# Kernel tuning notes

Measured on AMD Instinct MI355X. Metric: run time of the kernel, lower is better.

The kernel has to match this reference:

```python
import jax, jax.numpy as jnp
import numpy as np
from jax import lax

NUM_CLASSES = 80
CONF_THRE = 0.01   # testconf in source
NMS_THRE = 0.2     # nmsthresh in source
N = 8400           # YOLOX anchors at 640x640: 80^2+40^2+20^2
IMG = 640.0


def setup_inputs() -> dict:
    key = jax.random.key(0)
    pred = jax.random.uniform(key, (N, 5 + NUM_CLASSES), dtype=jnp.float32)
    # scale cx,cy,w,h to pixel units so boxes are realistic
    pred = pred.at[:, :4].multiply(IMG)
    return {"prediction": pred}


def _pairwise_iou(boxes):
    # boxes: [N,4] in x1,y1,x2,y2
    area = (boxes[:, 2] - boxes[:, 0]) * (boxes[:, 3] - boxes[:, 1])  # [N]
    lt = jnp.maximum(boxes[:, None, :2], boxes[None, :, :2])  # [N,N,2]
    rb = jnp.minimum(boxes[:, None, 2:], boxes[None, :, 2:])  # [N,N,2]
    wh = jnp.clip(rb - lt, 0.0)
    inter = wh[..., 0] * wh[..., 1]
    return inter / (area[:, None] + area[None, :] - inter + 1e-9)


def reference(prediction):
    # ---- box corner decode (cx,cy,w,h -> x1,y1,x2,y2) ----
    cx, cy, w, h = prediction[:, 0], prediction[:, 1], prediction[:, 2], prediction[:, 3]
    boxes = jnp.stack([cx - w / 2, cy - h / 2, cx + w / 2, cy + h / 2], axis=1)

    # ---- per-class max ----
    cls_scores = prediction[:, 5:5 + NUM_CLASSES]
    class_conf = jnp.max(cls_scores, axis=1, keepdims=True)            # [N,1]
    class_pred = jnp.argmax(cls_scores, axis=1).astype(prediction.dtype)[:, None]

    obj = prediction[:, 4]
    valid = obj >= CONF_THRE                                            # conf mask

    # detections = [x1,y1,x2,y2, obj_conf, class_conf, class_pred]  -> [N,7]
    det = jnp.concatenate([boxes, obj[:, None], class_conf, class_pred], axis=1)

    # ---- class-agnostic greedy NMS on obj score (fixed-shape version) ----
    scores = jnp.where(valid, obj, -1.0)
    order = jnp.argsort(-scores)
    det_s = det[order]
    boxes_s = boxes[order]
    valid_s = valid[order]

    iou = _pairwise_iou(boxes_s)  # [N,N] ~282MB, dominant traffic
    idx = jnp.arange(N)

    def step(keep, inp):
        i, row, v = inp
        alive = keep[i] & v                      # only a kept valid box suppresses
        supp = alive & (row > NMS_THRE) & (idx > i)
        return keep & ~supp, None

    keep0 = jnp.ones((N,), dtype=bool)
    keep, _ = lax.scan(step, keep0, (idx, iou, valid_s))
    keep = keep & valid_s

    # suppressed / below-conf rows are zeroed (torch returns a ragged subset;
    # here we return the score-sorted, mask-zeroed fixed-shape equivalent)
    out = det_s * keep[:, None].astype(det_s.dtype)
    return out
```

## Files before the change

kernel.cpp:

```cpp
#include <hip/hip_runtime.h>
#include <stdint.h>

#define N_BOX 8400
#define NCLS 80
#define PSTRIDE 85
#define NW 132
#define NTILE 8778
#define ZROWI N_BOX
#define CONF_T 0.01f
#define NMS_T 0.2f

typedef unsigned long long u64;

#define OFF_DET     0
#define OFF_DIAGT   0
#define OFF_SUP1    67584
#define OFF_SUP2    135168
#define OFF_SUP3    202752
#define OFF_KEYS    268800
#define OFF_DETS    336000
#define OFF_BOXESS  604800
#define OFF_MASK    739200
#define OFF_VCNT    9611712

__device__ __forceinline__ unsigned fmap_desc(float f) {
    unsigned u = __float_as_uint(f);
    unsigned m = (u & 0x80000000u) ? ~u : (u | 0x80000000u);
    return ~m;
}

__device__ __forceinline__ u64 readlane64(u64 v, int lane) {
    unsigned lo = (unsigned)__builtin_amdgcn_readlane((int)(unsigned)v, lane);
    unsigned hi = (unsigned)__builtin_amdgcn_readlane((int)(unsigned)(v >> 32), lane);
    return ((u64)hi << 32) | lo;
}

__device__ __forceinline__ u64 shfl_xor64(u64 v, int m) {
    int lo = __shfl_xor((int)(unsigned)v, m);
    int hi = __shfl_xor((int)(unsigned)(v >> 32), m);
    return ((u64)(unsigned)hi << 32) | (unsigned)lo;
}

__device__ __forceinline__ u64 bittranspose64(u64 x, int lane) {
    const u64 P0 = 0x5555555555555555ull, P1 = 0x3333333333333333ull,
              P2 = 0x0F0F0F0F0F0F0F0Full, P3 = 0x00FF00FF00FF00FFull,
              P4 = 0x0000FFFF0000FFFFull, P5 = 0x00000000FFFFFFFFull;
#define TSTEP(s, p) do {                                                 \
        u64 y = shfl_xor64(x, s);                                        \
        x = (lane & (s)) ? ((x & ~(p)) | ((y & ~(p)) >> (s)))            \
                         : ((x & (p))  | ((y & (p))  << (s)));           \
    } while (0)
    TSTEP(1, P0); TSTEP(2, P1); TSTEP(4, P2);
    TSTEP(8, P3); TSTEP(16, P4); TSTEP(32, P5);
#undef TSTEP
    return x;
}

__device__ __forceinline__ u64 wmask(int w, int V) {
    int nb = V - (w << 6);
    if (nb <= 0) return 0ull;
    if (nb >= 64) return ~0ull;
    return (1ull << nb) - 1ull;
}

__device__ __forceinline__ void step_barrier() {
    asm volatile("s_waitcnt lgkmcnt(0)" ::: "memory");
    __builtin_amdgcn_s_barrier();
    asm volatile("" ::: "memory");
}

__global__ __launch_bounds__(256) void prep_k(const float* __restrict__ pred,
                                              float* __restrict__ det,
                                              u64* __restrict__ keys,
                                              u64* __restrict__ mask) {
    if (blockIdx.x == 0 && threadIdx.x < NW)
        mask[(size_t)ZROWI * NW + threadIdx.x] = 0ull;
    int gt = blockIdx.x * 256 + threadIdx.x;
    int i = gt >> 2, q = gt & 3;
    if (i >= N_BOX) return;
    const float* p = pred + (size_t)i * PSTRIDE;
    int cbase = q * 20;
    float best = p[5 + cbase];
    int arg = cbase;
    for (int c = 1; c < 20; ++c) {
        float v = p[5 + cbase + c];
        if (v > best) { best = v; arg = cbase + c; }
    }
    for (int d = 1; d < 4; d <<= 1) {
        float ob = __shfl_xor(best, d);
        int   oa = __shfl_xor(arg, d);
        if (ob > best || (ob == best && oa < arg)) { best = ob; arg = oa; }
    }
    if (q == 0) {
        float cx = p[0], cy = p[1], w = p[2], h = p[3], obj = p[4];
        float hw = __fmul_rn(w, 0.5f), hh = __fmul_rn(h, 0.5f);
        float x1 = __fsub_rn(cx, hw), y1 = __fsub_rn(cy, hh);
        float x2 = __fadd_rn(cx, hw), y2 = __fadd_rn(cy, hh);
        bool valid = (obj >= CONF_T);
        float score = valid ? obj : -1.0f;
        keys[i] = ((u64)fmap_desc(score) << 32) | (unsigned)i;
        float4* dr = (float4*)(det + (size_t)i * 8);
        dr[0] = make_float4(x1, y1, x2, y2);
        dr[1] = make_float4(obj, best, (float)arg, 0.0f);
    }
}

__global__ __launch_bounds__(256) void rank_k(const u64* __restrict__ keys,
                                              const float* __restrict__ det,
                                              float4* __restrict__ det_s,
                                              float4* __restrict__ boxes_s,
                                              int* __restrict__ vcount) {
    int t = threadIdx.x;
    int i = blockIdx.x * 32 + (t & 31);
    int s = t >> 5;
    u64 my = (i < N_BOX) ? keys[i] : ~0ull;
    int cnt = 0, cv = 0;
    int j0 = s * 1050, j1 = j0 + 1050;
    for (int j = j0; j < j1; j += 2) {
        ulonglong2 kk = *(const ulonglong2*)(keys + j);
        cnt += (kk.x < my) + (kk.y < my);
        cv  += ((long long)kk.x >= 0) + ((long long)kk.y >= 0);
    }
    __shared__ int sc[256], sv[256];
    sc[t] = cnt; sv[t] = cv;
    __syncthreads();
    if (t < 32) {
        int r = sc[t] + sc[t + 32] + sc[t + 64] + sc[t + 96]
              + sc[t + 128] + sc[t + 160] + sc[t + 192] + sc[t + 224];
        if (i < N_BOX) {
            const float4* dr = (const float4*)(det + (size_t)i * 8);
            float4 b0 = dr[0], b1 = dr[1];
            det_s[(size_t)r * 2]     = b0;
            det_s[(size_t)r * 2 + 1] = b1;
            boxes_s[r] = b0;
        }
        if (blockIdx.x == 0 && t == 0) {
            *vcount = sv[0] + sv[32] + sv[64] + sv[96]
                    + sv[128] + sv[160] + sv[192] + sv[224];
        }
    }
}

__global__ __launch_bounds__(256) void mask_k(const float4* __restrict__ boxes_s,
                                              u64* __restrict__ mask,
                                              u64* __restrict__ diagT,
                                              u64* __restrict__ sup1,
                                              u64* __restrict__ sup2,
                                              u64* __restrict__ sup3) {
    int sub = threadIdx.x >> 6, lane = threadIdx.x & 63;
    int tt = blockIdx.x * 4 + sub;
    bool tv = (tt < NTILE);
    __shared__ float4 cB[4][64];
    __shared__ float  cA[4][64];
    int rb = 0, cb = 0;
    if (tv) {
        rb = (int)((2.0f * NW + 1.0f
                    - sqrtf((2.0f * NW + 1.0f) * (2.0f * NW + 1.0f) - 8.0f * (float)tt)) * 0.5f);
        while (rb > 0 && rb * NW - rb * (rb - 1) / 2 > tt) rb--;
        while ((rb + 1) * NW - (rb + 1) * rb / 2 <= tt) rb++;
        cb = rb + (tt - (rb * NW - rb * (rb - 1) / 2));
        int c0 = cb * 64 + lane;
        float4 b = (c0 < N_BOX) ? boxes_s[c0] : make_float4(0.f, 0.f, 0.f, 0.f);
        cB[sub][lane] = b;
        cA[sub][lane] = __fmul_rn(__fsub_rn(b.z, b.x), __fsub_rn(b.w, b.y));
    }
    __syncthreads();
    if (!tv) return;
    int r = rb * 64 + lane;
    bool inb = (r < N_BOX);
    float4 rx = boxes_s[inb ? r : (N_BOX - 1)];
    float ra = __fmul_rn(__fsub_rn(rx.z, rx.x), __fsub_rn(rx.w, rx.y));
    u64 bits = 0ull;
    int cbase = cb * 64;
    for (int j = 0; j < 64; ++j) {
        int c = cbase + j;
        if (c >= N_BOX || c <= r) continue;
        float4 cx4 = cB[sub][j];
        float ltx = fmaxf(rx.x, cx4.x), lty = fmaxf(rx.y, cx4.y);
        float rbx = fminf(rx.z, cx4.z), rby = fminf(rx.w, cx4.w);
        float wx = fmaxf(__fsub_rn(rbx, ltx), 0.0f);
        float wy = fmaxf(__fsub_rn(rby, lty), 0.0f);
        float inter = __fmul_rn(wx, wy);
        float denom = __fadd_rn(__fsub_rn(__fadd_rn(ra, cA[sub][j]), inter), 1e-9f);
        float iou = __fdiv_rn(inter, denom);
        if (iou > NMS_T) bits |= (1ull << j);
    }
    if (inb) mask[(size_t)r * NW + cb] = bits;
    int d = cb - rb;
    if (d <= 3) {
        u64 tb = bittranspose64(bits, lane);
        size_t idx = (size_t)cb * 64 + lane;
        if (d == 0)      diagT[idx] = tb;
        else if (d == 1) sup1[idx]  = tb;
        else if (d == 2) sup2[idx]  = tb;
        else             sup3[idx]  = tb;
    }
}

__global__ __launch_bounds__(256, 1) void scan_k(const u64* __restrict__ mask,
                                                 const u64* __restrict__ diagT,
                                                 const u64* __restrict__ sup1,
                                                 const u64* __restrict__ sup2,
                                                 const u64* __restrict__ sup3,
                                                 const int* __restrict__ vcount,
                                                 const float* __restrict__ det_s,
                                                 float* __restrict__ out) {
    __shared__ u64 remvP1[NW + 2];
    __shared__ u64 remvP2[NW + 2];
    __shared__ u64 Lbuf[NW];
    int tid = threadIdx.x, lane = tid & 63, wv = tid >> 6;
    int V = *vcount;
    for (int i = tid; i < NW + 2; i += 256) { remvP1[i] = 0ull; remvP2[i] = 0ull; }
    __syncthreads();

    if (wv == 0) {
        u64 A1 = 0ull, A2 = 0ull, A3 = 0ull;
        u64 d0P, s1P, s2P, s3P, d0Q, s1Q, s2Q, s3Q;
#define TL(S, kk) do {                                                   \
        int t_ = (kk) < NW ? (kk) : (NW - 1);                            \
        size_t ix_ = (size_t)t_ * 64 + lane;                             \
        d0##S = diagT[ix_]; s1##S = sup1[ix_];                           \
        s2##S = sup2[ix_];  s3##S = sup3[ix_];                           \
    } while (0)
#define STEP0(kk, S) do {                                                \
        int k_ = (kk);                                                   \
        u64 cur_ = remvP1[k_] | remvP2[k_];                              \
        cur_ |= __ballot((s1##S & A1) != 0ull);                          \
        cur_ |= __ballot((s2##S & A2) != 0ull);                          \
        cur_ |= __ballot((s3##S & A3) != 0ull);                          \
        u64 m_ = wmask(k_, V);                                           \
        u64 ns_ = (~cur_) & m_;                                          \
        u64 L_ = 0ull;                                                   \
        while (ns_) {                                                    \
            int b_ = __builtin_ctzll(ns_);                               \
            L_ |= 1ull << b_;                                            \
            u64 sup_ = __ballot((int)((d0##S >> b_) & 1ull));            \
            ns_ &= ~sup_;                                                \
            ns_ &= ~(1ull << b_);                                        \
        }                                                                \
        if (lane == 0) Lbuf[k_] = L_;                                    \
        A3 = A2; A2 = A1; A1 = L_;                                       \
        TL(S, k_ + 2);                                                   \
        step_barrier();                                                  \
    } while (0)
        TL(P, 0);
        TL(Q, 1);
        for (int c = 0; c < NW; c += 2) {
            STEP0(c + 0, P);
            STEP0(c + 1, Q);
        }
#undef STEP0
#undef TL
    } else if (wv <= 2) {
        int half = wv - 1;
        u64* myP = half ? remvP2 : remvP1;
        int tw = (lane < 4) ? (128 + lane) : 131;
        u64 Ra = 0ull, Rb = 0ull, Rc = 0ull;
        u64 Pa0=0,Pa1=0,Pa2=0,Pa3=0, Pb0=0,Pb1=0,Pb2=0,Pb3=0, Pc0=0,Pc1=0,Pc2=0,Pc3=0;
        u64 Qa0=0,Qa1=0,Qa2=0,Qa3=0, Qb0=0,Qb1=0,Qb2=0,Qb3=0, Qc0=0,Qc1=0,Qc2=0,Qc3=0;

#define CONS(S) do {                                                     \
        Ra |= (S##a0 | S##a1) | (S##a2 | S##a3);                         \
        Rb |= (S##b0 | S##b1) | (S##b2 | S##b3);                         \
        Rc |= (S##c0 | S##c1) | (S##c2 | S##c3);                         \
    } while (0)

#define LROW(S, i) do {                                                  \
        size_t ri_ = rem_ ? (size_t)(rbase_ + __builtin_ctz(rem_))       \
                          : (size_t)ZROWI;                               \
        rem_ &= rem_ - 1u;                                               \
        const u64* rp_ = mask + ri_ * NW;                                \
        ulonglong2 v_ = *(const ulonglong2*)(rp_ + 2 * lane);            \
        S##a##i = v_.x; S##b##i = v_.y; S##c##i = rp_[tw];               \
    } while (0)

#define STEP1(jj, S) do {                                                \
        int j_ = (jj);                                                   \
        CONS(S);                                  \
        int w_ = j_ + 1;                                                 \
        u64 rw_ = (w_ < 128) ? ((w_ & 1) ? Rb : Ra) : Rc;                \
        int sl_ = (w_ < 128) ? (w_ >> 1) : (w_ - 128);                   \
        u64 pv_ = readlane64(rw_, sl_);                                  \
        if (lane == 0) myP[w_] = pv_;                                    \
        u64 Lfull_ = (j_ >= 1) ? Lbuf[j_ - 1] : 0ull;                    \
        unsigned rem_ = half ? (unsigned)(Lfull_ >> 32)                  \
                             : (unsigned)Lfull_;                         \
        int rbase_ = ((j_ - 1) << 6) + 32 * half;                        \
        LROW(S, 0); LROW(S, 1); LROW(S, 2); LROW(S, 3);                  \
        while (rem_) {                              \
            u64 xa_ = 0, xb_ = 0, xc_ = 0;                               \
            for (int q_ = 0; q_ < 8; ++q_) {                             \
                size_t ri_ = rem_ ? (size_t)(rbase_ + __builtin_ctz(rem_)) \
                                  : (size_t)ZROWI;                       \
                rem_ &= rem_ - 1u;                                       \
                const u64* rp_ = mask + ri_ * NW;                        \
                ulonglong2 v_ = *(const ulonglong2*)(rp_ + 2 * lane);    \
                xa_ |= v_.x; xb_ |= v_.y; xc_ |= rp_[tw];                \
            }                                                            \
            Ra |= xa_; Rb |= xb_; Rc |= xc_;                             \
        }                                                                \
        step_barrier();                                                  \
    } while (0)

        for (int c = 0; c < NW; c += 2) {
            STEP1(c + 0, P);
            STEP1(c + 1, Q);
        }
#undef STEP1
#undef LROW
#undef CONS
    } else {
        const float4* ds = (const float4*)det_s;
        for (int c = 0; c < NW; ++c) {
            int i0 = c * 128 + lane;       i0 = i0 < 16800 ? i0 : 16799;
            int i1 = c * 128 + 64 + lane;  i1 = i1 < 16800 ? i1 : 16799;
            float4 a = ds[i0];
            float4 b = ds[i1];
            asm volatile("" :: "v"(a.x), "v"(b.x));
            step_barrier();
        }
    }

    __syncthreads();
    for (int r = tid; r < N_BOX; r += 256) {
        bool k = (Lbuf[r >> 6] >> (r & 63)) & 1ull;
        const float4* dr = (const float4*)(det_s + (size_t)r * 8);
        float4 b0 = dr[0], b1 = dr[1];
        float* op = out + (size_t)r * 7;
        op[0] = k ? b0.x : 0.0f;
        op[1] = k ? b0.y : 0.0f;
        op[2] = k ? b0.z : 0.0f;
        op[3] = k ? b0.w : 0.0f;
        op[4] = k ? b1.x : 0.0f;
        op[5] = k ? b1.y : 0.0f;
        op[6] = k ? b1.z : 0.0f;
    }
}

extern "C" void kernel_launch(void* const* d_in, const int* in_sizes, int n_in,
                              void* d_out, int out_size, void* d_ws, size_t ws_size,
                              hipStream_t stream) {
    const float* pred = (const float*)d_in[0];
    char* ws = (char*)d_ws;
    float*    det     = (float*)   (ws + OFF_DET);
    u64*      diagT   = (u64*)     (ws + OFF_DIAGT);
    u64*      sup1    = (u64*)     (ws + OFF_SUP1);
    u64*      sup2    = (u64*)     (ws + OFF_SUP2);
    u64*      sup3    = (u64*)     (ws + OFF_SUP3);
    u64*      keys    = (u64*)     (ws + OFF_KEYS);
    float*    det_s   = (float*)   (ws + OFF_DETS);
    float4*   boxes_s = (float4*)  (ws + OFF_BOXESS);
    u64*      mask    = (u64*)     (ws + OFF_MASK);
    int*      vcount  = (int*)     (ws + OFF_VCNT);

    prep_k<<<132, 256, 0, stream>>>(pred, det, keys, mask);
    rank_k<<<264, 256, 0, stream>>>(keys, det, (float4*)det_s, boxes_s, vcount);
    mask_k<<<(NTILE + 3) / 4, 256, 0, stream>>>(boxes_s, mask, diagT, sup1, sup2, sup3);
    scan_k<<<1, 256, 0, stream>>>(mask, diagT, sup1, sup2, sup3, vcount,
                                  det_s, (float*)d_out);
}
```

Measured before the change: 143.2 us.

## Process two column words per scan step with wider near-diagonal transposed bands

The single-block greedy NMS scan now resolves two 64-box words per barrier step instead of one, which halves the number of inter-wave barriers. To make this work, the mask kernel also stores transposed bands for diagonal offsets 4 and 5, and the resolver wave uses them for the extra lookback. The row-OR waves now gather rows from two words per step with deeper unrolling. The spare wave now writes the masked output rows as the scan proceeds instead of only prefetching, leaving a small tail for the final epilogue. Risks include higher register pressure, extra band writes in the mask kernel, and a longer serial chain inside each step.

```diff
diff --git a/kernel.cpp b/kernel.cpp
--- a/kernel.cpp
+++ b/kernel.cpp
@@ -5,6 +5,7 @@
 #define NCLS 80
 #define PSTRIDE 85
 #define NW 132
+#define NPAIR 66
 #define NTILE 8778
 #define ZROWI N_BOX
 #define CONF_T 0.01f
@@ -22,6 +23,8 @@
 #define OFF_BOXESS  604800
 #define OFF_MASK    739200
 #define OFF_VCNT    9611712
+#define OFF_SUP4    9611728
+#define OFF_SUP5    9679312
 
 __device__ __forceinline__ unsigned fmap_desc(float f) {
     unsigned u = __float_as_uint(f);
@@ -146,7 +149,9 @@
                                               u64* __restrict__ diagT,
                                               u64* __restrict__ sup1,
                                               u64* __restrict__ sup2,
-                                              u64* __restrict__ sup3) {
+                                              u64* __restrict__ sup3,
+                                              u64* __restrict__ sup4,
+                                              u64* __restrict__ sup5) {
     int sub = threadIdx.x >> 6, lane = threadIdx.x & 63;
     int tt = blockIdx.x * 4 + sub;
     bool tv = (tt < NTILE);
@@ -187,13 +192,15 @@
     }
     if (inb) mask[(size_t)r * NW + cb] = bits;
     int d = cb - rb;
-    if (d <= 3) {
+    if (d <= 5) {
         u64 tb = bittranspose64(bits, lane);
         size_t idx = (size_t)cb * 64 + lane;
         if (d == 0)      diagT[idx] = tb;
         else if (d == 1) sup1[idx]  = tb;
         else if (d == 2) sup2[idx]  = tb;
-        else             sup3[idx]  = tb;
+        else if (d == 3) sup3[idx]  = tb;
+        else if (d == 4) sup4[idx]  = tb;
+        else             sup5[idx]  = tb;
     }
 }
 
@@ -202,127 +209,178 @@
                                                  const u64* __restrict__ sup1,
                                                  const u64* __restrict__ sup2,
                                                  const u64* __restrict__ sup3,
+                                                 const u64* __restrict__ sup4,
+                                                 const u64* __restrict__ sup5,
                                                  const int* __restrict__ vcount,
                                                  const float* __restrict__ det_s,
                                                  float* __restrict__ out) {
-    __shared__ u64 remvP1[NW + 2];
-    __shared__ u64 remvP2[NW + 2];
+    __shared__ u64 remvP1[NW + 4];
+    __shared__ u64 remvP2[NW + 4];
     __shared__ u64 Lbuf[NW];
     int tid = threadIdx.x, lane = tid & 63, wv = tid >> 6;
     int V = *vcount;
-    for (int i = tid; i < NW + 2; i += 256) { remvP1[i] = 0ull; remvP2[i] = 0ull; }
+    for (int i = tid; i < NW + 4; i += 256) { remvP1[i] = 0ull; remvP2[i] = 0ull; }
+    for (int i = tid; i < NW; i += 256) Lbuf[i] = 0ull;
     __syncthreads();
 
     if (wv == 0) {
-        u64 A1 = 0ull, A2 = 0ull, A3 = 0ull;
-        u64 d0P, s1P, s2P, s3P, d0Q, s1Q, s2Q, s3Q;
-#define TL(S, kk) do {                                                   \
-        int t_ = (kk) < NW ? (kk) : (NW - 1);                            \
-        size_t ix_ = (size_t)t_ * 64 + lane;                             \
-        d0##S = diagT[ix_]; s1##S = sup1[ix_];                           \
-        s2##S = sup2[ix_];  s3##S = sup3[ix_];                           \
-    } while (0)
-#define STEP0(kk, S) do {                                                \
-        int k_ = (kk);                                                   \
-        u64 cur_ = remvP1[k_] | remvP2[k_];                              \
-        cur_ |= __ballot((s1##S & A1) != 0ull);                          \
-        cur_ |= __ballot((s2##S & A2) != 0ull);                          \
-        cur_ |= __ballot((s3##S & A3) != 0ull);                          \
-        u64 m_ = wmask(k_, V);                                           \
-        u64 ns_ = (~cur_) & m_;                                          \
-        u64 L_ = 0ull;                                                   \
+        u64 A1 = 0ull, A2 = 0ull, A3 = 0ull, A4 = 0ull;
+        u64 dEP,s1EP,s2EP,s3EP,s4EP, dOP,s1OP,s2OP,s3OP,s4OP,s5OP;
+        u64 dEQ,s1EQ,s2EQ,s3EQ,s4EQ, dOQ,s1OQ,s2OQ,s3OQ,s4OQ,s5OQ;
+#define TL(S, pp) do {                                                   \
+        int p_ = (pp) < NPAIR ? (pp) : (NPAIR - 1);                      \
+        size_t ex_ = (size_t)(2 * p_) * 64 + lane;                       \
+        size_t ox_ = ex_ + 64;                                           \
+        dE##S = diagT[ex_]; s1E##S = sup1[ex_]; s2E##S = sup2[ex_];      \
+        s3E##S = sup3[ex_]; s4E##S = sup4[ex_];                          \
+        dO##S = diagT[ox_]; s1O##S = sup1[ox_]; s2O##S = sup2[ox_];      \
+        s3O##S = sup3[ox_]; s4O##S = sup4[ox_]; s5O##S = sup5[ox_];      \
+    } while (0)
+#define RES(curv, dd, mm, Lout) do {                                     \
+        u64 ns_ = (~(curv)) & (mm);                                      \
+        Lout = 0ull;                                                     \
         while (ns_) {                                                    \
             int b_ = __builtin_ctzll(ns_);                               \
-            L_ |= 1ull << b_;                                            \
-            u64 sup_ = __ballot((int)((d0##S >> b_) & 1ull));            \
+            Lout |= 1ull << b_;                                          \
+            u64 sup_ = __ballot((int)((dd >> b_) & 1ull));               \
             ns_ &= ~sup_;                                                \
             ns_ &= ~(1ull << b_);                                        \
         }                                                                \
-        if (lane == 0) Lbuf[k_] = L_;                                    \
-        A3 = A2; A2 = A1; A1 = L_;                                       \
-        TL(S, k_ + 2);                                                   \
+    } while (0)
+#define STEP0(tt_, S) do {                                               \
+        int e_ = 2 * (tt_), o_ = e_ + 1;                                 \
+        u64 cur_ = remvP1[e_] | remvP2[e_];                              \
+        cur_ |= __ballot((s1E##S & A1) != 0ull);                         \
+        cur_ |= __ballot((s2E##S & A2) != 0ull);                         \
+        cur_ |= __ballot((s3E##S & A3) != 0ull);                         \
+        cur_ |= __ballot((s4E##S & A4) != 0ull);                         \
+        u64 Le_;                                                         \
+        RES(cur_, dE##S, wmask(e_, V), Le_);                             \
+        u64 curo_ = remvP1[o_] | remvP2[o_];                             \
+        curo_ |= __ballot((s1O##S & Le_) != 0ull);                       \
+        curo_ |= __ballot((s2O##S & A1) != 0ull);                        \
+        curo_ |= __ballot((s3O##S & A2) != 0ull);                        \
+        curo_ |= __ballot((s4O##S & A3) != 0ull);                        \
+        curo_ |= __ballot((s5O##S & A4) != 0ull);                        \
+        u64 Lo_;                                                         \
+        RES(curo_, dO##S, wmask(o_, V), Lo_);                            \
+        if (lane == 0) { Lbuf[e_] = Le_; Lbuf[o_] = Lo_; }               \
+        A4 = A2; A3 = A1; A2 = Le_; A1 = Lo_;                            \
+        TL(S, (tt_) + 2);                                                \
         step_barrier();                                                  \
     } while (0)
         TL(P, 0);
         TL(Q, 1);
-        for (int c = 0; c < NW; c += 2) {
-            STEP0(c + 0, P);
-            STEP0(c + 1, Q);
+        for (int t = 0; t < NPAIR; t += 2) {
+            STEP0(t, P);
+            STEP0(t + 1, Q);
         }
 #undef STEP0
+#undef RES
 #undef TL
     } else if (wv <= 2) {
         int half = wv - 1;
         u64* myP = half ? remvP2 : remvP1;
         int tw = (lane < 4) ? (128 + lane) : 131;
         u64 Ra = 0ull, Rb = 0ull, Rc = 0ull;
-        u64 Pa0=0,Pa1=0,Pa2=0,Pa3=0, Pb0=0,Pb1=0,Pb2=0,Pb3=0, Pc0=0,Pc1=0,Pc2=0,Pc3=0;
-        u64 Qa0=0,Qa1=0,Qa2=0,Qa3=0, Qb0=0,Qb1=0,Qb2=0,Qb3=0, Qc0=0,Qc1=0,Qc2=0,Qc3=0;
+        u64 Pa0=0,Pa1=0,Pa2=0,Pa3=0,Pa4=0,Pa5=0,Pa6=0,Pa7=0;
+        u64 Pb0=0,Pb1=0,Pb2=0,Pb3=0,Pb4=0,Pb5=0,Pb6=0,Pb7=0;
+        u64 Pc0=0,Pc1=0,Pc2=0,Pc3=0,Pc4=0,Pc5=0,Pc6=0,Pc7=0;
+        u64 Qa0=0,Qa1=0,Qa2=0,Qa3=0,Qa4=0,Qa5=0,Qa6=0,Qa7=0;
+        u64 Qb0=0,Qb1=0,Qb2=0,Qb3=0,Qb4=0,Qb5=0,Qb6=0,Qb7=0;
+        u64 Qc0=0,Qc1=0,Qc2=0,Qc3=0,Qc4=0,Qc5=0,Qc6=0,Qc7=0;
 
 #define CONS(S) do {                                                     \
-        Ra |= (S##a0 | S##a1) | (S##a2 | S##a3);                         \
-        Rb |= (S##b0 | S##b1) | (S##b2 | S##b3);                         \
-        Rc |= (S##c0 | S##c1) | (S##c2 | S##c3);                         \
-    } while (0)
-
-#define LROW(S, i) do {                                                  \
-        size_t ri_ = rem_ ? (size_t)(rbase_ + __builtin_ctz(rem_))       \
-                          : (size_t)ZROWI;                               \
-        rem_ &= rem_ - 1u;                                               \
+        Ra |= ((S##a0|S##a1)|(S##a2|S##a3))|((S##a4|S##a5)|(S##a6|S##a7));\
+        Rb |= ((S##b0|S##b1)|(S##b2|S##b3))|((S##b4|S##b5)|(S##b6|S##b7));\
+        Rc |= ((S##c0|S##c1)|(S##c2|S##c3))|((S##c4|S##c5)|(S##c6|S##c7));\
+    } while (0)
+
+#define PUB(w_) do {                                                     \
+        u64 rw_ = ((w_) < 128) ? (((w_) & 1) ? Rb : Ra) : Rc;            \
+        int sl_ = ((w_) < 128) ? ((w_) >> 1) : ((w_) - 128);             \
+        u64 pv_ = readlane64(rw_, sl_);                                  \
+        if (lane == 0) myP[w_] = pv_;                                    \
+    } while (0)
+
+#define LROW(S, i, remv_, rbase_) do {                                   \
+        size_t ri_ = (remv_) ? (size_t)((rbase_) + __builtin_ctz(remv_)) \
+                             : (size_t)ZROWI;                            \
+        (remv_) &= (remv_) - 1u;                                         \
         const u64* rp_ = mask + ri_ * NW;                                \
         ulonglong2 v_ = *(const ulonglong2*)(rp_ + 2 * lane);            \
         S##a##i = v_.x; S##b##i = v_.y; S##c##i = rp_[tw];               \
     } while (0)
 
-#define STEP1(jj, S) do {                                                \
-        int j_ = (jj);                                                   \
-        CONS(S);                                  \
-        int w_ = j_ + 1;                                                 \
-        u64 rw_ = (w_ < 128) ? ((w_ & 1) ? Rb : Ra) : Rc;                \
-        int sl_ = (w_ < 128) ? (w_ >> 1) : (w_ - 128);                   \
-        u64 pv_ = readlane64(rw_, sl_);                                  \
-        if (lane == 0) myP[w_] = pv_;                                    \
-        u64 Lfull_ = (j_ >= 1) ? Lbuf[j_ - 1] : 0ull;                    \
-        unsigned rem_ = half ? (unsigned)(Lfull_ >> 32)                  \
-                             : (unsigned)Lfull_;                         \
-        int rbase_ = ((j_ - 1) << 6) + 32 * half;                        \
-        LROW(S, 0); LROW(S, 1); LROW(S, 2); LROW(S, 3);                  \
-        while (rem_) {                              \
+#define XTRA(remv_, rbase_) do {                                         \
+        while (remv_) {                                                  \
             u64 xa_ = 0, xb_ = 0, xc_ = 0;                               \
             for (int q_ = 0; q_ < 8; ++q_) {                             \
-                size_t ri_ = rem_ ? (size_t)(rbase_ + __builtin_ctz(rem_)) \
-                                  : (size_t)ZROWI;                       \
-                rem_ &= rem_ - 1u;                                       \
+                size_t ri_ = (remv_) ? (size_t)((rbase_) + __builtin_ctz(remv_)) \
+                                     : (size_t)ZROWI;                    \
+                (remv_) &= (remv_) - 1u;                                 \
                 const u64* rp_ = mask + ri_ * NW;                        \
                 ulonglong2 v_ = *(const ulonglong2*)(rp_ + 2 * lane);    \
                 xa_ |= v_.x; xb_ |= v_.y; xc_ |= rp_[tw];                \
             }                                                            \
             Ra |= xa_; Rb |= xb_; Rc |= xc_;                             \
         }                                                                \
+    } while (0)
+
+#define STEP1(tt_, Siss, Scon) do {                                      \
+        int t_ = (tt_);                                                  \
+        CONS(Scon);                       \
+        PUB(2 * t_ + 2);                                                 \
+        PUB(2 * t_ + 3);                                                 \
+        u64 Le_ = (t_ >= 1) ? Lbuf[2 * t_ - 2] : 0ull;                   \
+        u64 Lo_ = (t_ >= 1) ? Lbuf[2 * t_ - 1] : 0ull;                   \
+        unsigned re_ = half ? (unsigned)(Le_ >> 32) : (unsigned)Le_;     \
+        unsigned ro_ = half ? (unsigned)(Lo_ >> 32) : (unsigned)Lo_;     \
+        int rbe_ = ((2 * t_ - 2) << 6) + 32 * half;                      \
+        int rbo_ = rbe_ + 64;                                            \
+        LROW(Siss, 0, re_, rbe_); LROW(Siss, 1, re_, rbe_);              \
+        LROW(Siss, 2, re_, rbe_); LROW(Siss, 3, re_, rbe_);              \
+        LROW(Siss, 4, ro_, rbo_); LROW(Siss, 5, ro_, rbo_);              \
+        LROW(Siss, 6, ro_, rbo_); LROW(Siss, 7, ro_, rbo_);              \
+        XTRA(re_, rbe_);                                                 \
+        XTRA(ro_, rbo_);                                                 \
         step_barrier();                                                  \
     } while (0)
 
-        for (int c = 0; c < NW; c += 2) {
-            STEP1(c + 0, P);
-            STEP1(c + 1, Q);
+        for (int t = 0; t < NPAIR; t += 2) {
+            STEP1(t, P, Q);
+            STEP1(t + 1, Q, P);
         }
 #undef STEP1
+#undef XTRA
 #undef LROW
+#undef PUB
 #undef CONS
     } else {
-        const float4* ds = (const float4*)det_s;
-        for (int c = 0; c < NW; ++c) {
-            int i0 = c * 128 + lane;       i0 = i0 < 16800 ? i0 : 16799;
-            int i1 = c * 128 + 64 + lane;  i1 = i1 < 16800 ? i1 : 16799;
-            float4 a = ds[i0];
-            float4 b = ds[i1];
-            asm volatile("" :: "v"(a.x), "v"(b.x));
+        for (int t = 0; t < NPAIR; ++t) {
+            if (t >= 1) {
+                int r0 = (2 * t - 2) * 64 + lane;
+                int r1 = r0 + 64;
+                bool k0 = (Lbuf[2 * t - 2] >> lane) & 1ull;
+                bool k1 = (Lbuf[2 * t - 1] >> lane) & 1ull;
+                const float4* d0 = (const float4*)(det_s + (size_t)r0 * 8);
+                const float4* d1 = (const float4*)(det_s + (size_t)r1 * 8);
+                float4 a0 = d0[0], a1 = d0[1], b0 = d1[0], b1 = d1[1];
+                float* o0 = out + (size_t)r0 * 7;
+                float* o1 = out + (size_t)r1 * 7;
+                o0[0]=k0?a0.x:0.f; o0[1]=k0?a0.y:0.f; o0[2]=k0?a0.z:0.f;
+                o0[3]=k0?a0.w:0.f; o0[4]=k0?a1.x:0.f; o0[5]=k0?a1.y:0.f;
+                o0[6]=k0?a1.z:0.f;
+                o1[0]=k1?b0.x:0.f; o1[1]=k1?b0.y:0.f; o1[2]=k1?b0.z:0.f;
+                o1[3]=k1?b0.w:0.f; o1[4]=k1?b1.x:0.f; o1[5]=k1?b1.y:0.f;
+                o1[6]=k1?b1.z:0.f;
+            }
             step_barrier();
         }
     }
 
     __syncthreads();
-    for (int r = tid; r < N_BOX; r += 256) {
+    for (int r = 8320 + tid; r < N_BOX; r += 256) {
         bool k = (Lbuf[r >> 6] >> (r & 63)) & 1ull;
         const float4* dr = (const float4*)(det_s + (size_t)r * 8);
         float4 b0 = dr[0], b1 = dr[1];
@@ -347,6 +405,8 @@
     u64*      sup1    = (u64*)     (ws + OFF_SUP1);
     u64*      sup2    = (u64*)     (ws + OFF_SUP2);
     u64*      sup3    = (u64*)     (ws + OFF_SUP3);
+    u64*      sup4    = (u64*)     (ws + OFF_SUP4);
+    u64*      sup5    = (u64*)     (ws + OFF_SUP5);
     u64*      keys    = (u64*)     (ws + OFF_KEYS);
     float*    det_s   = (float*)   (ws + OFF_DETS);
     float4*   boxes_s = (float4*)  (ws + OFF_BOXESS);
@@ -355,7 +415,8 @@
 
     prep_k<<<132, 256, 0, stream>>>(pred, det, keys, mask);
     rank_k<<<264, 256, 0, stream>>>(keys, det, (float4*)det_s, boxes_s, vcount);
-    mask_k<<<(NTILE + 3) / 4, 256, 0, stream>>>(boxes_s, mask, diagT, sup1, sup2, sup3);
-    scan_k<<<1, 256, 0, stream>>>(mask, diagT, sup1, sup2, sup3, vcount,
-                                  det_s, (float*)d_out);
-}
+    mask_k<<<(NTILE + 3) / 4, 256, 0, stream>>>(boxes_s, mask, diagT, sup1, sup2,
+                                                sup3, sup4, sup5);
+    scan_k<<<1, 256, 0, stream>>>(mask, diagT, sup1, sup2, sup3, sup4, sup5,
+                                  vcount, det_s, (float*)d_out);
+}
```

After: 138.6 us. 1.03x faster.
